# Performance work log

Hardware: AMD Instinct MI355X
Metric: run time of the kernel (lower is better)

## Reference

```python
import jax, jax.numpy as jnp
import numpy as np

N_GROUPS = 20   # hard-coded batch_size in NeRFGraph.forward
K = 3           # knn_graph k
IN_XYZ = 63
SKIP = 4
D = 8


def setup_inputs() -> dict:
    key = jax.random.key(0)
    B, W = 40960, 256
    G = B // N_GROUPS
    ks = jax.random.split(key, 22)

    def p(k, shape):
        fan_in = shape[-2] if len(shape) >= 2 else shape[-1]
        return jax.random.normal(k, shape, dtype=jnp.float32) / np.sqrt(fan_in)

    # batch assignment: exactly G nodes per group, randomly shuffled
    # (faithful to the np.zeros/fill/shuffle logic in the torch forward)
    batch_ids = jax.random.permutation(ks[1], jnp.repeat(jnp.arange(N_GROUPS, dtype=jnp.int32), G))

    return {
        "x": jax.random.normal(ks[0], (B, IN_XYZ + 27), dtype=jnp.float32),
        "batch_ids": batch_ids,
        "w0": p(ks[2], (IN_XYZ, W)), "b0": p(ks[3], (W,)),
        "w_mid": p(ks[4], (6, W, W)), "b_mid": p(ks[5], (6, W)),       # layers 1,2,3,5,6,7
        "w_skip": p(ks[6], (W + IN_XYZ, W)), "b_skip": p(ks[7], (W,)),  # layer 4 (skip)
        "w_final": p(ks[8], (W, W)), "b_final": p(ks[9], (W,)),
        "w_sigma": p(ks[10], (W, 1)), "b_sigma": p(ks[11], (1,)),
        "e1_w1": p(ks[12], (2 * (W + 27), W // 2)), "e1_b1": p(ks[13], (W // 2,)),
        "e1_w2": p(ks[14], (W // 2, W // 2)), "e1_b2": p(ks[15], (W // 2,)),
        "e2_w1": p(ks[16], (W, W // 2)), "e2_b1": p(ks[17], (W // 2,)),
        "e2_w2": p(ks[18], (W // 2, W // 2)), "e2_b2": p(ks[19], (W // 2,)),
        "w_rgb": p(ks[20], (W // 2, 3)), "b_rgb": p(ks[21], (3,)),
    }


def _knn(xyz, batch_ids):
    """k-NN within each of the N_GROUPS equal-size groups (loop=False).
    Returns (B, K) global neighbor indices for each node."""
    B = xyz.shape[0]
    G = B // N_GROUPS
    perm = jnp.argsort(batch_ids)                 # group nodes contiguously
    xg = xyz[perm].reshape(N_GROUPS, G, -1)
    sq = jnp.sum(xg * xg, axis=-1)                # (NG, G)
    d2 = sq[:, :, None] + sq[:, None, :] - 2.0 * jnp.einsum('gic,gjc->gij', xg, xg)
    d2 = jnp.where(jnp.eye(G, dtype=bool)[None], jnp.inf, d2)  # loop=False
    nbr_local = jax.lax.top_k(-d2, K)[1]          # (NG, G, K) local indices
    perm_g = perm.reshape(N_GROUPS, G)
    nbr_glob = jax.vmap(lambda p_, n_: p_[n_])(perm_g, nbr_local)  # (NG, G, K)
    inv = jnp.argsort(perm)
    return nbr_glob.reshape(B, K)[inv]


def _edge_conv(feat, nbr, w1, b1, w2, b2):
    # message: MLP(cat[x_i, x_j - x_i]); aggr='mean' over exactly K neighbors
    xi = feat[:, None, :]                         # (B, 1, C)
    xj = feat[nbr]                                # (B, K, C) gather
    tmp = jnp.concatenate([jnp.broadcast_to(xi, xj.shape), xj - xi], axis=-1)
    h = jax.nn.relu(tmp @ w1 + b1)
    h = jax.nn.relu(h @ w2 + b2)
    return h.mean(axis=1)                         # scatter-mean == mean over K


def reference(x, batch_ids, w0, b0, w_mid, b_mid, w_skip, b_skip, w_final, b_final,
              w_sigma, b_sigma, e1_w1, e1_b1, e1_w2, e1_b2, e2_w1, e2_b1, e2_w2, e2_b2,
              w_rgb, b_rgb):
    input_xyz, input_dir = x[:, :IN_XYZ], x[:, IN_XYZ:]
    nbr = _knn(input_xyz, batch_ids)
    h = jax.nn.relu(input_xyz @ w0 + b0)
    m = 0
    for i in range(1, D):
        if i == SKIP:
            h = jax.nn.relu(jnp.concatenate([input_xyz, h], axis=-1) @ w_skip + b_skip)
        else:
            h = jax.nn.relu(h @ w_mid[m] + b_mid[m])
            m += 1
    sigma = h @ w_sigma + b_sigma                  # (B, 1)
    feat = h @ w_final + b_final                   # xyz_encoding_final (no ReLU)
    d = _edge_conv(jnp.concatenate([feat, input_dir], axis=-1), nbr, e1_w1, e1_b1, e1_w2, e1_b2)
    d = _edge_conv(d, nbr, e2_w1, e2_b1, e2_w2, e2_b2)
    rgb = jax.nn.sigmoid(d @ w_rgb + b_rgb)        # (B, 3)
    return jnp.concatenate([rgb, sigma], axis=-1)  # (B, 4)
```

## Files before the change

kernel.cpp:

```cpp
#include <hip/hip_runtime.h>
#include <hip/hip_bf16.h>
#include <math.h>

#define B_TOTAL 40960
#define NGRP 20
#define GSZ 2048
#define CPART 4

typedef short short8 __attribute__((ext_vector_type(8)));
typedef short short4v __attribute__((ext_vector_type(4)));
typedef float f32x4 __attribute__((ext_vector_type(4)));
typedef float f32x16 __attribute__((ext_vector_type(16)));
typedef _Float16 half8 __attribute__((ext_vector_type(8)));
typedef _Float16 half4 __attribute__((ext_vector_type(4)));

__device__ __forceinline__ unsigned short bf16rne(float v)
{
    unsigned int u = __float_as_uint(v);
    unsigned int r = (u + 0x7FFFu + ((u >> 16) & 1u)) >> 16;
    return (unsigned short)r;
}

__device__ __forceinline__ float bf2f(unsigned short h)
{
    return __uint_as_float((unsigned int)h << 16);
}

__device__ __forceinline__ void splitf16(const float* v, half8& hi, half8& lo)
{
    #pragma unroll
    for (int j = 0; j < 8; j++) {
        _Float16 h = (_Float16)v[j];
        hi[j] = h;
        lo[j] = (_Float16)(v[j] - (float)h);
    }
}

__device__ __forceinline__ unsigned int fkey(float f)
{
    unsigned int u = __float_as_uint(f);
    unsigned int m = (unsigned int)((int)u >> 31) | 0x80000000u;
    return u ^ m;
}

__device__ __forceinline__ void ins3p(unsigned int k, unsigned int i,
    unsigned int& k0, unsigned int& i0, unsigned int& k1, unsigned int& i1,
    unsigned int& k2, unsigned int& i2)
{
    bool c0 = k < k0;
    unsigned int tk = c0 ? k0 : k, ti = c0 ? i0 : i;
    k0 = c0 ? k : k0;  i0 = c0 ? i : i0;
    bool c1 = tk < k1;
    unsigned int sk = c1 ? k1 : tk, si = c1 ? i1 : ti;
    k1 = c1 ? tk : k1; i1 = c1 ? ti : i1;
    bool c2 = sk < k2;
    k2 = c2 ? sk : k2; i2 = c2 ? si : i2;
}

__device__ __forceinline__ void mergerow(unsigned int& k0, unsigned int& i0,
    unsigned int& k1, unsigned int& i1, unsigned int& k2, unsigned int& i2)
{
    #pragma unroll
    for (int m = 1; m <= 8; m <<= 1) {
        unsigned int ok0 = (unsigned int)__shfl_xor((int)k0, m);
        unsigned int oi0 = (unsigned int)__shfl_xor((int)i0, m);
        unsigned int ok1 = (unsigned int)__shfl_xor((int)k1, m);
        unsigned int oi1 = (unsigned int)__shfl_xor((int)i1, m);
        unsigned int ok2 = (unsigned int)__shfl_xor((int)k2, m);
        unsigned int oi2 = (unsigned int)__shfl_xor((int)i2, m);
        ins3p(ok0, oi0, k0, i0, k1, i1, k2, i2);
        ins3p(ok1, oi1, k0, i0, k1, i1, k2, i2);
        ins3p(ok2, oi2, k0, i0, k1, i1, k2, i2);
    }
}

__global__ __launch_bounds__(1024) void k_scatter_det(const int* __restrict__ bid,
                                                      int* __restrict__ grp)
{
    __shared__ int cnts[640];
    __shared__ int offs[640];
    const int tid = threadIdx.x;
    const int w = tid >> 6, lane = tid & 63;
    const int g = blockIdx.x;
    for (int c = 0; c < 40; c++) {
        int i = c * 1024 + tid;
        unsigned long long m = __ballot(bid[i] == g);
        if (lane == 0) cnts[c * 16 + w] = __popcll(m);
    }
    __syncthreads();
    if (w == 0) {
        int base = lane * 10;
        int loc[10];
        int s = 0;
        #pragma unroll
        for (int u = 0; u < 10; u++) { loc[u] = s; s += cnts[base + u]; }
        int incl = s;
        #pragma unroll
        for (int d = 1; d < 64; d <<= 1) {
            int t = __shfl_up(incl, d);
            if (lane >= d) incl += t;
        }
        int excl = incl - s;
        #pragma unroll
        for (int u = 0; u < 10; u++) offs[base + u] = excl + loc[u];
    }
    __syncthreads();
    for (int c = 0; c < 40; c++) {
        int i = c * 1024 + tid;
        bool f = (bid[i] == g);
        unsigned long long m = __ballot(f);
        unsigned long long below = (lane == 0) ? 0ull : (m << (64 - lane)) >> (64 - lane);
        below = m & ((lane == 63) ? 0x7FFFFFFFFFFFFFFFull : ((1ull << lane) - 1ull));
        if (f) grp[g * GSZ + offs[c * 16 + w] + __popcll(below)] = i;
    }
}

__device__ __forceinline__ void do_wprep_trunk(int t, const float* __restrict__ w0,
    const float* __restrict__ wmid, const float* __restrict__ wskip,
    const float* __restrict__ wfin, _Float16* __restrict__ wfrag)
{
    const int CUMa[10] = {0,4,20,36,52,72,88,104,120,136};
    const int KCa[9]   = {4,16,16,16,20,16,16,16,16};
    int q = t >> 12;
    int L = 0;
    #pragma unroll
    for (int i = 0; i < 9; i++) if (q >= CUMa[i + 1]) L = i + 1;
    int cum = 0, kcn = 16;
    #pragma unroll
    for (int i = 0; i < 9; i++) if (L == i) { cum = CUMa[i]; kcn = KCa[i]; }
    int u = t - (cum << 12);
    int j = u & 7, lane = (u >> 3) & 63;
    int ckk = u >> 9;
    int kc = ckk % kcn, ct = ckk / kcn;
    int col = ct * 32 + (lane & 31);
    int k = kc * 16 + ((lane >> 5) << 3) + j;
    float w;
    if (L == 0)      w = (k < 63)  ? w0[k * 256 + col] : 0.f;
    else if (L == 4) w = (k < 256) ? wskip[(63 + k) * 256 + col]
                       : (k < 319) ? wskip[(k - 256) * 256 + col] : 0.f;
    else if (L == 8) w = wfin[k * 256 + col];
    else {
        int m = (L <= 3) ? (L - 1) : (L - 2);
        w = wmid[(size_t)m * 65536 + k * 256 + col];
    }
    wfrag[((size_t)cum << 12) + (size_t)ckk * 512 + lane * 8 + j] = (_Float16)w;
}

__device__ __forceinline__ void do_wprep_pq(int t, const float* __restrict__ src,
    int K, int KCN, _Float16* __restrict__ dst)
{
    int j = t & 7, lane = (t >> 3) & 63;
    int ckk = t >> 9;
    int kc = ckk % KCN, ct = ckk / KCN;
    int col = ct * 32 + (lane & 31);
    int k = kc * 16 + ((lane >> 5) << 3) + j;
    float w = 0.f;
    if (k < K) w = (col < 128) ? src[(size_t)k * 128 + col]
                               : src[(size_t)(K + k) * 128 + (col - 128)];
    dst[(size_t)ckk * 512 + lane * 8 + j] = (_Float16)w;
}

__device__ __forceinline__ void do_wprep_sq(int t, const float* __restrict__ src,
    _Float16* __restrict__ dst)
{
    int j = t & 7, lane = (t >> 3) & 63;
// ... 10 lines not shown
                       const float* __restrict__ e1w1, _Float16* __restrict__ wfpq1,
                       const float* __restrict__ e2w1, _Float16* __restrict__ wfpq2,
                       const float* __restrict__ e1w2, _Float16* __restrict__ wfe1,
                       const float* __restrict__ e2w2, _Float16* __restrict__ wfe2)
{
    const int b = blockIdx.x;
    const int tid = threadIdx.x;
    if (b < 2176) {
        do_wprep_trunk(b * 256 + tid, w0, wmid, wskip, wfin, wfrag);
    } else if (b < 2464) {
        do_wprep_pq((b - 2176) * 256 + tid, e1w1, 283, 18, wfpq1);
    } else if (b < 2592) {
        do_wprep_pq((b - 2464) * 256 + tid, e2w1, 128, 8, wfpq2);
    } else if (b < 2656) {
        do_wprep_sq((b - 2592) * 256 + tid, e1w2, wfe1);
    } else {
        do_wprep_sq((b - 2656) * 256 + tid, e2w2, wfe2);
    }
}

__global__ __launch_bounds__(256) void k_gather(const float* __restrict__ x,
    const int* __restrict__ grp, unsigned short* __restrict__ xbh,
    unsigned short* __restrict__ xbl, float* __restrict__ cn)
{
    __shared__ float tile[128][65];
    __shared__ int ids[128];
    const int tid = threadIdx.x;
    const int g = blockIdx.y;
    const int q0 = blockIdx.x * 128;
    if (tid < 128) ids[tid] = grp[g * GSZ + q0 + tid];
    __syncthreads();
    for (int s = tid; s < 128 * 64; s += 256) {
        int q = s >> 6, d = s & 63;
        tile[q][d] = (d < 63) ? x[(size_t)ids[q] * 90 + d] : 0.f;
    }
    __syncthreads();
    if (tid < 128) {
        float a = 0.f;
        #pragma unroll
        for (int d = 0; d < 63; d++) a = fmaf(tile[tid][d], tile[tid][d], a);
        cn[g * GSZ + q0 + tid] = a;
    }
    for (int s = tid; s < 128 * 32; s += 256) {
        int q = s >> 5, dp = (s & 31) << 1;
        float v0 = tile[q][dp], v1 = tile[q][dp + 1];
        unsigned short h0 = bf16rne(v0), h1 = bf16rne(v1);
        unsigned short l0 = bf16rne(v0 - bf2f(h0)), l1 = bf16rne(v1 - bf2f(h1));
        size_t pt = (size_t)g * GSZ + q0 + q;
        ((unsigned int*)xbh)[pt * 32 + (dp >> 1)] = (unsigned int)h0 | ((unsigned int)h1 << 16);
        ((unsigned int*)xbl)[pt * 32 + (dp >> 1)] = (unsigned int)l0 | ((unsigned int)l1 << 16);
    }
}

__global__ __launch_bounds__(256) void k_knn_mfma(const unsigned short* __restrict__ xbh,
    const unsigned short* __restrict__ xbl, const float* __restrict__ cn,
    unsigned long long* __restrict__ pkey)
{
    __shared__ char cbuf[2][16384];
    const int tid = threadIdx.x;
    const int lane = tid & 63;
    const int wave = tid >> 6;
    const int g = blockIdx.z;
    const int part = blockIdx.y;
    const int qt0 = blockIdx.x * 64 + wave * 16;
    const size_t gbase = (size_t)g * GSZ;
    const int lp = lane & 15;
    const int kgrp = lane >> 4;
    const int kg = kgrp << 3;

    const size_t qb = (gbase + qt0 + lp) * 64;
    short8 ah0 = *(const short8*)(xbh + qb + kg);
    short8 ah1 = *(const short8*)(xbh + qb + 32 + kg);
    short8 al0 = *(const short8*)(xbl + qb + kg);
    short8 al1 = *(const short8*)(xbl + qb + 32 + kg);

    const int qp0 = qt0 + (kgrp << 2);

    unsigned int K00 = ~0u, I00 = 0, K01 = ~0u, I01 = 0, K02 = ~0u, I02 = 0;
    unsigned int K10 = ~0u, I10 = 0, K11 = ~0u, I11 = 0, K12 = ~0u, I12 = 0;
    unsigned int K20 = ~0u, I20 = 0, K21 = ~0u, I21 = 0, K22 = ~0u, I22 = 0;
    unsigned int K30 = ~0u, I30 = 0, K31 = ~0u, I31 = 0, K32 = ~0u, I32 = 0;

    const int scand = tid & 63;
    const int cbeg = part * (GSZ / CPART);
    const int s0 = wave, s1 = 4 + wave, s2 = 8 + wave, s3 = 12 + wave;
    const unsigned short* pl0 = (s0 < 8) ? xbh : xbl;
    const unsigned short* pl1 = (s1 < 8) ? xbh : xbl;
    const unsigned short* pl2 = (s2 < 8) ? xbh : xbl;
    const unsigned short* pl3 = (s3 < 8) ? xbh : xbl;

    short8 st0, st1, st2, st3;
    {
        size_t cb = (gbase + cbeg + scand) * 64;
        st0 = *(const short8*)(pl0 + cb + (s0 & 7) * 8);
        st1 = *(const short8*)(pl1 + cb + (s1 & 7) * 8);
        st2 = *(const short8*)(pl2 + cb + (s2 & 7) * 8);
        st3 = *(const short8*)(pl3 + cb + (s3 & 7) * 8);
    }
    *(short8*)&cbuf[0][(s0 << 10) + (scand << 4)] = st0;
    *(short8*)&cbuf[0][(s1 << 10) + (scand << 4)] = st1;
    *(short8*)&cbuf[0][(s2 << 10) + (scand << 4)] = st2;
    *(short8*)&cbuf[0][(s3 << 10) + (scand << 4)] = st3;

    for (int ch = 0; ch < 8; ch++) {
        const int cur = ch & 1;
        __syncthreads();
        if (ch < 7) {
            size_t cb = (gbase + cbeg + (ch + 1) * 64 + scand) * 64;
            st0 = *(const short8*)(pl0 + cb + (s0 & 7) * 8);
            st1 = *(const short8*)(pl1 + cb + (s1 & 7) * 8);
            st2 = *(const short8*)(pl2 + cb + (s2 & 7) * 8);
            st3 = *(const short8*)(pl3 + cb + (s3 & 7) * 8);
        }
        const int cc0 = cbeg + ch * 64;
        #pragma unroll
        for (int ct = 0; ct < 4; ct++) {
            const int coff = ((ct * 16 + lp) << 4);
            short8 bh0 = *(const short8*)&cbuf[cur][((kgrp)      << 10) + coff];
            short8 bh1 = *(const short8*)&cbuf[cur][((4 + kgrp)  << 10) + coff];
            short8 bl0 = *(const short8*)&cbuf[cur][((8 + kgrp)  << 10) + coff];
            short8 bl1 = *(const short8*)&cbuf[cur][((12 + kgrp) << 10) + coff];
            f32x4 acc = {0.f, 0.f, 0.f, 0.f};
            acc = __builtin_amdgcn_mfma_f32_16x16x32_bf16(ah0, bh0, acc, 0, 0, 0);
            acc = __builtin_amdgcn_mfma_f32_16x16x32_bf16(ah1, bh1, acc, 0, 0, 0);
            acc = __builtin_amdgcn_mfma_f32_16x16x32_bf16(al0, bh0, acc, 0, 0, 0);
            acc = __builtin_amdgcn_mfma_f32_16x16x32_bf16(al1, bh1, acc, 0, 0, 0);
            acc = __builtin_amdgcn_mfma_f32_16x16x32_bf16(ah0, bl0, acc, 0, 0, 0);
            acc = __builtin_amdgcn_mfma_f32_16x16x32_bf16(ah1, bl1, acc, 0, 0, 0);
            const float cnv = cn[gbase + cc0 + ct * 16 + lp];
            const int cpos = cc0 + ct * 16 + lp;
            const unsigned int ci = (unsigned int)cpos;
            {
                unsigned int k = fkey(fmaf(-2.f, acc[0], cnv));
                k = (cpos == qp0 + 0) ? 0xFFFFFFFFu : k;
                ins3p(k, ci, K00, I00, K01, I01, K02, I02);
            }
            {
                unsigned int k = fkey(fmaf(-2.f, acc[1], cnv));
                k = (cpos == qp0 + 1) ? 0xFFFFFFFFu : k;
                ins3p(k, ci, K10, I10, K11, I11, K12, I12);
            }
            {
                unsigned int k = fkey(fmaf(-2.f, acc[2], cnv));
                k = (cpos == qp0 + 2) ? 0xFFFFFFFFu : k;
                ins3p(k, ci, K20, I20, K21, I21, K22, I22);
            }
            {
                unsigned int k = fkey(fmaf(-2.f, acc[3], cnv));
                k = (cpos == qp0 + 3) ? 0xFFFFFFFFu : k;
                ins3p(k, ci, K30, I30, K31, I31, K32, I32);
            }
        }
        if (ch < 7) {
            *(short8*)&cbuf[cur ^ 1][(s0 << 10) + (scand << 4)] = st0;
            *(short8*)&cbuf[cur ^ 1][(s1 << 10) + (scand << 4)] = st1;
            *(short8*)&cbuf[cur ^ 1][(s2 << 10) + (scand << 4)] = st2;
            *(short8*)&cbuf[cur ^ 1][(s3 << 10) + (scand << 4)] = st3;
        }
    }

    mergerow(K00, I00, K01, I01, K02, I02);
    mergerow(K10, I10, K11, I11, K12, I12);
    mergerow(K20, I20, K21, I21, K22, I22);
    mergerow(K30, I30, K31, I31, K32, I32);

    if (lp == 0) {
        size_t ob = (gbase + (size_t)qp0) * (CPART * 3) + part * 3;
        pkey[ob + 0]  = ((unsigned long long)K00 << 32) | I00;
        pkey[ob + 1]  = ((unsigned long long)K01 << 32) | I01;
        pkey[ob + 2]  = ((unsigned long long)K02 << 32) | I02;
        pkey[ob + 12] = ((unsigned long long)K10 << 32) | I10;
        pkey[ob + 13] = ((unsigned long long)K11 << 32) | I11;
        pkey[ob + 14] = ((unsigned long long)K12 << 32) | I12;
        pkey[ob + 24] = ((unsigned long long)K20 << 32) | I20;
        pkey[ob + 25] = ((unsigned long long)K21 << 32) | I21;
        pkey[ob + 26] = ((unsigned long long)K22 << 32) | I22;
        pkey[ob + 36] = ((unsigned long long)K30 << 32) | I30;
        pkey[ob + 37] = ((unsigned long long)K31 << 32) | I31;
        pkey[ob + 38] = ((unsigned long long)K32 << 32) | I32;
    }
}

__device__ __forceinline__ void ins3u(unsigned long long k,
    unsigned long long& k0, unsigned long long& k1, unsigned long long& k2)
{
    if (k < k0)      { k2 = k1; k1 = k0; k0 = k; }
    else if (k < k1) { k2 = k1; k1 = k; }
    else if (k < k2) { k2 = k; }
}

__global__ void k_knn_merge(const unsigned long long* __restrict__ pkey,
                            const int* __restrict__ grp, int* __restrict__ nbr)
{
    int t = blockIdx.x * 256 + threadIdx.x;
    if (t >= NGRP * GSZ) return;
    int g = t >> 11;
    unsigned long long k0 = ~0ull, k1 = ~0ull, k2 = ~0ull;
    const unsigned long long* pk = pkey + (size_t)t * (CPART * 3);
    #pragma unroll
    for (int r = 0; r < CPART * 3; r++) ins3u(pk[r], k0, k1, k2);
    int qi = grp[t];
    nbr[(size_t)qi * 3 + 0] = grp[(g << 11) + (int)(k0 & 0xFFFFFFFFull)];
    nbr[(size_t)qi * 3 + 1] = grp[(g << 11) + (int)(k1 & 0xFFFFFFFFull)];
    nbr[(size_t)qi * 3 + 2] = grp[(g << 11) + (int)(k2 & 0xFFFFFFFFull)];
}

template<int KCH, int KCX, int OUTMODE>
__device__ __forceinline__ void mlayer64(_Float16 (*Hh)[264], _Float16 (*Hl)[264],
    int rowbase, const float* __restrict__ x, const _Float16* __restrict__ wl,
    const float* __restrict__ bias, int lane, int wave)
{
    const int r31 = lane & 31, g = lane >> 5;
    constexpr int KC = KCH + KCX;
    const int ct = wave;
    f32x16 acc0, acc1;
    #pragma unroll
    for (int r = 0; r < 16; r++) { acc0[r] = 0.f; acc1[r] = 0.f; }
    const _Float16* wp = wl + (size_t)ct * KC * 512 + lane * 8;
    #pragma unroll
    for (int kc = 0; kc < KCH; kc++) {
        half8 ah0 = *(const half8*)&Hh[r31][kc * 16 + g * 8];
        half8 al0 = *(const half8*)&Hl[r31][kc * 16 + g * 8];
        half8 ah1 = *(const half8*)&Hh[32 + r31][kc * 16 + g * 8];
        half8 al1 = *(const half8*)&Hl[32 + r31][kc * 16 + g * 8];
        half8 b = *(const half8*)(wp + kc * 512);
        acc0 = __builtin_amdgcn_mfma_f32_32x32x16_f16(ah0, b, acc0, 0, 0, 0);
        acc1 = __builtin_amdgcn_mfma_f32_32x32x16_f16(ah1, b, acc1, 0, 0, 0);
        acc0 = __builtin_amdgcn_mfma_f32_32x32x16_f16(al0, b, acc0, 0, 0, 0);
        acc1 = __builtin_amdgcn_mfma_f32_32x32x16_f16(al1, b, acc1, 0, 0, 0);
    }
    #pragma unroll
    for (int t = 0; t < KCX; t++) {
        const int kc = KCH + t;
        float v0[8], v1[8];
        #pragma unroll
        for (int j = 0; j < 8; j++) {
            int kx = t * 16 + g * 8 + j;
            v0[j] = (kx < 63) ? x[(size_t)(rowbase + r31) * 90 + kx] : 0.f;
            v1[j] = (kx < 63) ? x[(size_t)(rowbase + 32 + r31) * 90 + kx] : 0.f;
        }
        half8 xh0, xl0, xh1, xl1;
        splitf16(v0, xh0, xl0);
        splitf16(v1, xh1, xl1);
        half8 b = *(const half8*)(wp + kc * 512);
        acc0 = __builtin_amdgcn_mfma_f32_32x32x16_f16(xh0, b, acc0, 0, 0, 0);
        acc1 = __builtin_amdgcn_mfma_f32_32x32x16_f16(xh1, b, acc1, 0, 0, 0);
        acc0 = __builtin_amdgcn_mfma_f32_32x32x16_f16(xl0, b, acc0, 0, 0, 0);
        acc1 = __builtin_amdgcn_mfma_f32_32x32x16_f16(xl1, b, acc1, 0, 0, 0);
    }
    const float bv = bias[ct * 32 + r31];
    __syncthreads();
    #pragma unroll
    for (int r = 0; r < 16; r++) {
        int row = (r & 3) + 8 * (r >> 2) + 4 * g;
        float v0 = acc0[r] + bv;
        float v1 = acc1[r] + bv;
        if (OUTMODE == 0) { v0 = fmaxf(v0, 0.f); v1 = fmaxf(v1, 0.f); }
        _Float16 h0 = (_Float16)v0, h1 = (_Float16)v1;
        Hh[row][ct * 32 + r31] = h0;
        Hl[row][ct * 32 + r31] = (_Float16)(v0 - (float)h0);
        Hh[32 + row][ct * 32 + r31] = h1;
        Hl[32 + row][ct * 32 + r31] = (_Float16)(v1 - (float)h1);
    }
    __syncthreads();
}

__global__ __launch_bounds__(512, 4) void k_trunk_mfma(const float* __restrict__ x,
    const _Float16* __restrict__ wfrag,
    const float* __restrict__ b0, const float* __restrict__ bmid,
    const float* __restrict__ bskip, const float* __restrict__ bfin,
    const float* __restrict__ wsig, const float* __restrict__ bsig,
    const _Float16* __restrict__ wfpq1, float* __restrict__ PQ,
    float* __restrict__ out)
{
    __shared__ _Float16 Hh[64][264];
    __shared__ _Float16 Hl[64][264];
    __shared__ _Float16 Dh[64][40];
    __shared__ _Float16 Dl[64][40];
    const int tid = threadIdx.x;
    const int lane = tid & 63;
    const int wave = tid >> 6;
    const int r31 = lane & 31, g = lane >> 5;
    const int rowbase = blockIdx.x * 64;
    for (int s = tid; s < 64 * 32; s += 512) {
        int r = s >> 5, d = s & 31;
        float v = (d < 27) ? x[(size_t)(rowbase + r) * 90 + 63 + d] : 0.f;
        _Float16 h = (_Float16)v;
        Dh[r][d] = h;
        Dl[r][d] = (_Float16)(v - (float)h);
    }
    const _Float16* W = wfrag;
    mlayer64<0, 4, 0>(Hh, Hl, rowbase, x, W + (size_t)0   * 4096, b0,          lane, wave);
    mlayer64<16,0, 0>(Hh, Hl, rowbase, x, W + (size_t)4   * 4096, bmid + 0,    lane, wave);
    mlayer64<16,0, 0>(Hh, Hl, rowbase, x, W + (size_t)20  * 4096, bmid + 256,  lane, wave);
    mlayer64<16,0, 0>(Hh, Hl, rowbase, x, W + (size_t)36  * 4096, bmid + 512,  lane, wave);
    mlayer64<16,4, 0>(Hh, Hl, rowbase, x, W + (size_t)52  * 4096, bskip,       lane, wave);
    mlayer64<16,0, 0>(Hh, Hl, rowbase, x, W + (size_t)72  * 4096, bmid + 768,  lane, wave);
    mlayer64<16,0, 0>(Hh, Hl, rowbase, x, W + (size_t)88  * 4096, bmid + 1024, lane, wave);
    mlayer64<16,0, 0>(Hh, Hl, rowbase, x, W + (size_t)104 * 4096, bmid + 1280, lane, wave);
    if (wave < 2) {
        const int row = wave * 32 + r31;
        float s = 0.f;
        #pragma unroll
        for (int kk = 0; kk < 32; kk++) {
            half4 hh = *(const half4*)&Hh[row][g * 128 + kk * 4];
            half4 hl = *(const half4*)&Hl[row][g * 128 + kk * 4];
            float4 wv = *(const float4*)&wsig[g * 128 + kk * 4];
            s = fmaf((float)hh[0] + (float)hl[0], wv.x, s);
            s = fmaf((float)hh[1] + (float)hl[1], wv.y, s);
            s = fmaf((float)hh[2] + (float)hl[2], wv.z, s);
            s = fmaf((float)hh[3] + (float)hl[3], wv.w, s);
        }
        s += __shfl_xor(s, 32);
        if (lane < 32) out[(size_t)(rowbase + row) * 4 + 3] = s + bsig[0];
    }
    mlayer64<16,0, 2>(Hh, Hl, rowbase, x, W + (size_t)120 * 4096, bfin, lane, wave);
    {
        const int ct = wave;
        f32x16 p0, p1;
        #pragma unroll
        for (int r = 0; r < 16; r++) { p0[r] = 0.f; p1[r] = 0.f; }
        const _Float16* wp = wfpq1 + (size_t)ct * 18 * 512 + lane * 8;
        #pragma unroll
        for (int kc = 0; kc < 16; kc++) {
            half8 ah0 = *(const half8*)&Hh[r31][kc * 16 + g * 8];
            half8 al0 = *(const half8*)&Hl[r31][kc * 16 + g * 8];
            half8 ah1 = *(const half8*)&Hh[32 + r31][kc * 16 + g * 8];
            half8 al1 = *(const half8*)&Hl[32 + r31][kc * 16 + g * 8];
            half8 b = *(const half8*)(wp + kc * 512);
            p0 = __builtin_amdgcn_mfma_f32_32x32x16_f16(ah0, b, p0, 0, 0, 0);
            p1 = __builtin_amdgcn_mfma_f32_32x32x16_f16(ah1, b, p1, 0, 0, 0);
            p0 = __builtin_amdgcn_mfma_f32_32x32x16_f16(al0, b, p0, 0, 0, 0);
            p1 = __builtin_amdgcn_mfma_f32_32x32x16_f16(al1, b, p1, 0, 0, 0);
        }
        #pragma unroll
        for (int kc = 16; kc < 18; kc++) {
            const int dc = (kc - 16) * 16 + g * 8;
            half8 ah0 = *(const half8*)&Dh[r31][dc];
            half8 al0 = *(const half8*)&Dl[r31][dc];
            half8 ah1 = *(const half8*)&Dh[32 + r31][dc];
            half8 al1 = *(const half8*)&Dl[32 + r31][dc];
            half8 b = *(const half8*)(wp + kc * 512);
            p0 = __builtin_amdgcn_mfma_f32_32x32x16_f16(ah0, b, p0, 0, 0, 0);
            p1 = __builtin_amdgcn_mfma_f32_32x32x16_f16(ah1, b, p1, 0, 0, 0);
            p0 = __builtin_amdgcn_mfma_f32_32x32x16_f16(al0, b, p0, 0, 0, 0);
            p1 = __builtin_amdgcn_mfma_f32_32x32x16_f16(al1, b, p1, 0, 0, 0);
        }
        #pragma unroll
        for (int r = 0; r < 16; r++) {
            int row = (r & 3) + 8 * (r >> 2) + 4 * g;
            PQ[(size_t)(rowbase + row) * 256 + ct * 32 + r31] = p0[r];
            PQ[(size_t)(rowbase + 32 + row) * 256 + ct * 32 + r31] = p1[r];
        }
    }
}

template<int RGB>
__global__ __launch_bounds__(256) void k_edge_mfma(const float* __restrict__ PQ,
    const float* __restrict__ b1, const _Float16* __restrict__ wf2,
    const float* __restrict__ b2, const int* __restrict__ nbr,
    const _Float16* __restrict__ wfpq2, float* __restrict__ pqout,
    const float* __restrict__ wrgb, const float* __restrict__ brgb,
    float* __restrict__ out)
{
    __shared__ _Float16 Hh[128][136];
    __shared__ _Float16 Hl[128][136];
    const int tid = threadIdx.x;
    const int lane = tid & 63, wave = tid >> 6;
    const int r31 = lane & 31, g = lane >> 5;
    const int n0 = blockIdx.x * 32;

    for (int s = tid; s < 128 * 32; s += 256) {
        int e = s >> 5, c4 = (s & 31) << 2;
        int n = e >> 2, jj = e & 3;
        half4 zh = {(_Float16)0.f, (_Float16)0.f, (_Float16)0.f, (_Float16)0.f};
        if (jj < 3) {
            int i = n0 + n;
            int j = nbr[(size_t)i * 3 + jj];
            float4 p  = *(const float4*)&PQ[(size_t)i * 256 + c4];
            float4 qi = *(const float4*)&PQ[(size_t)i * 256 + 128 + c4];
            float4 qj = *(const float4*)&PQ[(size_t)j * 256 + 128 + c4];
            float4 bv = *(const float4*)&b1[c4];
            float v[4];
            v[0] = fmaxf(p.x + bv.x + qj.x - qi.x, 0.f);
            v[1] = fmaxf(p.y + bv.y + qj.y - qi.y, 0.f);
            v[2] = fmaxf(p.z + bv.z + qj.z - qi.z, 0.f);
            v[3] = fmaxf(p.w + bv.w + qj.w - qi.w, 0.f);
            half4 hh, hl;
            #pragma unroll
            for (int u = 0; u < 4; u++) {
                _Float16 h = (_Float16)v[u];
                hh[u] = h;
                hl[u] = (_Float16)(v[u] - (float)h);
            }
            *(half4*)&Hh[e][c4] = hh;
            *(half4*)&Hl[e][c4] = hl;
        } else {
            *(half4*)&Hh[e][c4] = zh;
            *(half4*)&Hl[e][c4] = zh;
        }
    }
    __syncthreads();

    const int ct = wave;
    f32x16 a0, a1, a2, a3;
    #pragma unroll
    for (int r = 0; r < 16; r++) { a0[r] = 0.f; a1[r] = 0.f; a2[r] = 0.f; a3[r] = 0.f; }
// ... 87 lines not shown
    }
}

extern "C" void kernel_launch(void* const* d_in, const int* in_sizes, int n_in,
                              void* d_out, int out_size, void* d_ws, size_t ws_size,
                              hipStream_t stream)
{
    const float* x     = (const float*)d_in[0];
    const int*   bid   = (const int*)d_in[1];
    const float* w0    = (const float*)d_in[2];
    const float* b0    = (const float*)d_in[3];
    const float* wmid  = (const float*)d_in[4];
    const float* bmid  = (const float*)d_in[5];
    const float* wskip = (const float*)d_in[6];
    const float* bskip = (const float*)d_in[7];
    const float* wfin  = (const float*)d_in[8];
    const float* bfin  = (const float*)d_in[9];
    const float* wsig  = (const float*)d_in[10];
    const float* bsig  = (const float*)d_in[11];
    const float* e1w1  = (const float*)d_in[12];
    const float* e1b1  = (const float*)d_in[13];
    const float* e1w2  = (const float*)d_in[14];
    const float* e1b2  = (const float*)d_in[15];
    const float* e2w1  = (const float*)d_in[16];
    const float* e2b1  = (const float*)d_in[17];
    const float* e2w2  = (const float*)d_in[18];
    const float* e2b2  = (const float*)d_in[19];
    const float* wrgb  = (const float*)d_in[20];
    const float* brgb  = (const float*)d_in[21];
    float* out = (float*)d_out;

    char* ws = (char*)d_ws;
    int* grp = (int*)(ws + 256);
    int* nbr = (int*)(ws + 164096);
    _Float16* wfpq1 = (_Float16*)(ws + 655616);
    _Float16* wfpq2 = (_Float16*)(ws + 950528);
    _Float16* wfe1  = (_Float16*)(ws + 1081600);
    _Float16* wfe2  = (_Float16*)(ws + 1147136);
    float* bufA = (float*)(ws + (2 << 20));
    float* bufB = bufA + (size_t)B_TOTAL * 256;

    unsigned short* xbh = (unsigned short*)bufA;
    unsigned short* xbl = xbh + (size_t)B_TOTAL * 64;
    float* cn   = (float*)(xbl + (size_t)B_TOTAL * 64);
    unsigned long long* pkey = (unsigned long long*)(cn + B_TOTAL);
    _Float16* wfrag = (_Float16*)((char*)bufA + ((size_t)20 << 20));
    float* PQ  = bufB;
    float* PQ2 = bufA;

    k_prep<<<2720, 256, 0, stream>>>(w0, wmid, wskip, wfin, wfrag,
                                     e1w1, wfpq1, e2w1, wfpq2, e1w2, wfe1, e2w2, wfe2);
    k_scatter_det<<<NGRP, 1024, 0, stream>>>(bid, grp);
    k_gather<<<dim3(GSZ / 128, NGRP), 256, 0, stream>>>(x, grp, xbh, xbl, cn);
    k_knn_mfma<<<dim3(GSZ / 64, CPART, NGRP), 256, 0, stream>>>(xbh, xbl, cn, pkey);
    k_knn_merge<<<(NGRP * GSZ + 255) / 256, 256, 0, stream>>>(pkey, grp, nbr);
    k_trunk_mfma<<<B_TOTAL / 64, 512, 0, stream>>>(x, wfrag, b0, bmid, bskip, bfin,
                                                   wsig, bsig, wfpq1, PQ, out);
    k_edge_mfma<0><<<B_TOTAL / 32, 256, 0, stream>>>(PQ, e1b1, wfe1, e1b2, nbr,
                                                     wfpq2, PQ2, nullptr, nullptr, nullptr);
    k_edge_mfma<1><<<B_TOTAL / 32, 256, 0, stream>>>(PQ2, e2b1, wfe2, e2b2, nbr,
                                                     nullptr, nullptr, wrgb, brgb, out);
}
```

Baseline: 347.3 us.

## Merge kNN and trunk MLP into one heterogeneous launch to run concurrently

```diff
diff --git a/kernel.cpp b/kernel.cpp
--- a/kernel.cpp
+++ b/kernel.cpp
@@ -8,7 +8,6 @@
 #define CPART 4
 
 typedef short short8 __attribute__((ext_vector_type(8)));
-typedef short short4v __attribute__((ext_vector_type(4)));
 typedef float f32x4 __attribute__((ext_vector_type(4)));
 typedef float f32x16 __attribute__((ext_vector_type(16)));
 typedef _Float16 half8 __attribute__((ext_vector_type(8)));
@@ -109,8 +108,8 @@
         int i = c * 1024 + tid;
         bool f = (bid[i] == g);
         unsigned long long m = __ballot(f);
-        unsigned long long below = (lane == 0) ? 0ull : (m << (64 - lane)) >> (64 - lane);
-        below = m & ((lane == 63) ? 0x7FFFFFFFFFFFFFFFull : ((1ull << lane) - 1ull));
+        unsigned long long below = m & ((lane == 63) ? 0x7FFFFFFFFFFFFFFFull
+                                                     : ((1ull << lane) - 1ull));
         if (f) grp[g * GSZ + offs[c * 16 + w] + __popcll(below)] = i;
     }
 }
@@ -227,159 +226,6 @@
     }
 }
 
-__global__ __launch_bounds__(256) void k_knn_mfma(const unsigned short* __restrict__ xbh,
-    const unsigned short* __restrict__ xbl, const float* __restrict__ cn,
-    unsigned long long* __restrict__ pkey)
-{
-    __shared__ char cbuf[2][16384];
-    const int tid = threadIdx.x;
-    const int lane = tid & 63;
-    const int wave = tid >> 6;
-    const int g = blockIdx.z;
-    const int part = blockIdx.y;
-    const int qt0 = blockIdx.x * 64 + wave * 16;
-    const size_t gbase = (size_t)g * GSZ;
-    const int lp = lane & 15;
-    const int kgrp = lane >> 4;
-    const int kg = kgrp << 3;
-
-    const size_t qb = (gbase + qt0 + lp) * 64;
-    short8 ah0 = *(const short8*)(xbh + qb + kg);
-    short8 ah1 = *(const short8*)(xbh + qb + 32 + kg);
-    short8 al0 = *(const short8*)(xbl + qb + kg);
-    short8 al1 = *(const short8*)(xbl + qb + 32 + kg);
-
-    const int qp0 = qt0 + (kgrp << 2);
-
-    unsigned int K00 = ~0u, I00 = 0, K01 = ~0u, I01 = 0, K02 = ~0u, I02 = 0;
-    unsigned int K10 = ~0u, I10 = 0, K11 = ~0u, I11 = 0, K12 = ~0u, I12 = 0;
-    unsigned int K20 = ~0u, I20 = 0, K21 = ~0u, I21 = 0, K22 = ~0u, I22 = 0;
-    unsigned int K30 = ~0u, I30 = 0, K31 = ~0u, I31 = 0, K32 = ~0u, I32 = 0;
-
-    const int scand = tid & 63;
-    const int cbeg = part * (GSZ / CPART);
-    const int s0 = wave, s1 = 4 + wave, s2 = 8 + wave, s3 = 12 + wave;
-    const unsigned short* pl0 = (s0 < 8) ? xbh : xbl;
-    const unsigned short* pl1 = (s1 < 8) ? xbh : xbl;
-    const unsigned short* pl2 = (s2 < 8) ? xbh : xbl;
-    const unsigned short* pl3 = (s3 < 8) ? xbh : xbl;
-
-    short8 st0, st1, st2, st3;
-    {
-        size_t cb = (gbase + cbeg + scand) * 64;
-        st0 = *(const short8*)(pl0 + cb + (s0 & 7) * 8);
-        st1 = *(const short8*)(pl1 + cb + (s1 & 7) * 8);
-        st2 = *(const short8*)(pl2 + cb + (s2 & 7) * 8);
-        st3 = *(const short8*)(pl3 + cb + (s3 & 7) * 8);
-    }
-    *(short8*)&cbuf[0][(s0 << 10) + (scand << 4)] = st0;
-    *(short8*)&cbuf[0][(s1 << 10) + (scand << 4)] = st1;
-    *(short8*)&cbuf[0][(s2 << 10) + (scand << 4)] = st2;
-    *(short8*)&cbuf[0][(s3 << 10) + (scand << 4)] = st3;
-
-    for (int ch = 0; ch < 8; ch++) {
-        const int cur = ch & 1;
-        __syncthreads();
-        if (ch < 7) {
-            size_t cb = (gbase + cbeg + (ch + 1) * 64 + scand) * 64;
-            st0 = *(const short8*)(pl0 + cb + (s0 & 7) * 8);
-            st1 = *(const short8*)(pl1 + cb + (s1 & 7) * 8);
-            st2 = *(const short8*)(pl2 + cb + (s2 & 7) * 8);
-            st3 = *(const short8*)(pl3 + cb + (s3 & 7) * 8);
-        }
-        const int cc0 = cbeg + ch * 64;
-        #pragma unroll
-        for (int ct = 0; ct < 4; ct++) {
-            const int coff = ((ct * 16 + lp) << 4);
-            short8 bh0 = *(const short8*)&cbuf[cur][((kgrp)      << 10) + coff];
-            short8 bh1 = *(const short8*)&cbuf[cur][((4 + kgrp)  << 10) + coff];
-            short8 bl0 = *(const short8*)&cbuf[cur][((8 + kgrp)  << 10) + coff];
-            short8 bl1 = *(const short8*)&cbuf[cur][((12 + kgrp) << 10) + coff];
-            f32x4 acc = {0.f, 0.f, 0.f, 0.f};
-            acc = __builtin_amdgcn_mfma_f32_16x16x32_bf16(ah0, bh0, acc, 0, 0, 0);
-            acc = __builtin_amdgcn_mfma_f32_16x16x32_bf16(ah1, bh1, acc, 0, 0, 0);
-            acc = __builtin_amdgcn_mfma_f32_16x16x32_bf16(al0, bh0, acc, 0, 0, 0);
-            acc = __builtin_amdgcn_mfma_f32_16x16x32_bf16(al1, bh1, acc, 0, 0, 0);
-            acc = __builtin_amdgcn_mfma_f32_16x16x32_bf16(ah0, bl0, acc, 0, 0, 0);
-            acc = __builtin_amdgcn_mfma_f32_16x16x32_bf16(ah1, bl1, acc, 0, 0, 0);
-            const float cnv = cn[gbase + cc0 + ct * 16 + lp];
-            const int cpos = cc0 + ct * 16 + lp;
-            const unsigned int ci = (unsigned int)cpos;
-            {
-                unsigned int k = fkey(fmaf(-2.f, acc[0], cnv));
-                k = (cpos == qp0 + 0) ? 0xFFFFFFFFu : k;
-                ins3p(k, ci, K00, I00, K01, I01, K02, I02);
-            }
-            {
-                unsigned int k = fkey(fmaf(-2.f, acc[1], cnv));
-                k = (cpos == qp0 + 1) ? 0xFFFFFFFFu : k;
-                ins3p(k, ci, K10, I10, K11, I11, K12, I12);
-            }
-            {
-                unsigned int k = fkey(fmaf(-2.f, acc[2], cnv));
-                k = (cpos == qp0 + 2) ? 0xFFFFFFFFu : k;
-                ins3p(k, ci, K20, I20, K21, I21, K22, I22);
-            }
-            {
-                unsigned int k = fkey(fmaf(-2.f, acc[3], cnv));
-                k = (cpos == qp0 + 3) ? 0xFFFFFFFFu : k;
-                ins3p(k, ci, K30, I30, K31, I31, K32, I32);
-            }
-        }
-        if (ch < 7) {
-            *(short8*)&cbuf[cur ^ 1][(s0 << 10) + (scand << 4)] = st0;
-            *(short8*)&cbuf[cur ^ 1][(s1 << 10) + (scand << 4)] = st1;
-            *(short8*)&cbuf[cur ^ 1][(s2 << 10) + (scand << 4)] = st2;
-            *(short8*)&cbuf[cur ^ 1][(s3 << 10) + (scand << 4)] = st3;
-        }
-    }
-
-    mergerow(K00, I00, K01, I01, K02, I02);
-    mergerow(K10, I10, K11, I11, K12, I12);
-    mergerow(K20, I20, K21, I21, K22, I22);
-    mergerow(K30, I30, K31, I31, K32, I32);
-
-    if (lp == 0) {
-        size_t ob = (gbase + (size_t)qp0) * (CPART * 3) + part * 3;
-        pkey[ob + 0]  = ((unsigned long long)K00 << 32) | I00;
-        pkey[ob + 1]  = ((unsigned long long)K01 << 32) | I01;
-        pkey[ob + 2]  = ((unsigned long long)K02 << 32) | I02;
-        pkey[ob + 12] = ((unsigned long long)K10 << 32) | I10;
-        pkey[ob + 13] = ((unsigned long long)K11 << 32) | I11;
-        pkey[ob + 14] = ((unsigned long long)K12 << 32) | I12;
-        pkey[ob + 24] = ((unsigned long long)K20 << 32) | I20;
-        pkey[ob + 25] = ((unsigned long long)K21 << 32) | I21;
-        pkey[ob + 26] = ((unsigned long long)K22 << 32) | I22;
-        pkey[ob + 36] = ((unsigned long long)K30 << 32) | I30;
-        pkey[ob + 37] = ((unsigned long long)K31 << 32) | I31;
-        pkey[ob + 38] = ((unsigned long long)K32 << 32) | I32;
-    }
-}
-
-__device__ __forceinline__ void ins3u(unsigned long long k,
-    unsigned long long& k0, unsigned long long& k1, unsigned long long& k2)
-{
-    if (k < k0)      { k2 = k1; k1 = k0; k0 = k; }
-    else if (k < k1) { k2 = k1; k1 = k; }
-    else if (k < k2) { k2 = k; }
-}
-
-__global__ void k_knn_merge(const unsigned long long* __restrict__ pkey,
-                            const int* __restrict__ grp, int* __restrict__ nbr)
-{
-    int t = blockIdx.x * 256 + threadIdx.x;
-    if (t >= NGRP * GSZ) return;
-    int g = t >> 11;
-    unsigned long long k0 = ~0ull, k1 = ~0ull, k2 = ~0ull;
-    const unsigned long long* pk = pkey + (size_t)t * (CPART * 3);
-    #pragma unroll
-    for (int r = 0; r < CPART * 3; r++) ins3u(pk[r], k0, k1, k2);
-    int qi = grp[t];
-    nbr[(size_t)qi * 3 + 0] = grp[(g << 11) + (int)(k0 & 0xFFFFFFFFull)];
-    nbr[(size_t)qi * 3 + 1] = grp[(g << 11) + (int)(k1 & 0xFFFFFFFFull)];
-    nbr[(size_t)qi * 3 + 2] = grp[(g << 11) + (int)(k2 & 0xFFFFFFFFull)];
-}
-
 template<int KCH, int KCX, int OUTMODE>
 __device__ __forceinline__ void mlayer64(_Float16 (*Hh)[264], _Float16 (*Hl)[264],
     int rowbase, const float* __restrict__ x, const _Float16* __restrict__ wl,
@@ -440,94 +286,236 @@
     __syncthreads();
 }
 
-__global__ __launch_bounds__(512, 4) void k_trunk_mfma(const float* __restrict__ x,
+__global__ __launch_bounds__(512, 4) void k_main(const float* __restrict__ x,
     const _Float16* __restrict__ wfrag,
     const float* __restrict__ b0, const float* __restrict__ bmid,
     const float* __restrict__ bskip, const float* __restrict__ bfin,
     const float* __restrict__ wsig, const float* __restrict__ bsig,
     const _Float16* __restrict__ wfpq1, float* __restrict__ PQ,
-    float* __restrict__ out)
-{
-    __shared__ _Float16 Hh[64][264];
-    __shared__ _Float16 Hl[64][264];
-    __shared__ _Float16 Dh[64][40];
-    __shared__ _Float16 Dl[64][40];
+    float* __restrict__ out,
+    const unsigned short* __restrict__ xbh, const unsigned short* __restrict__ xbl,
+    const float* __restrict__ cn, unsigned long long* __restrict__ pkey)
+{
+    __shared__ union SM {
+        struct { _Float16 Hh[64][264]; _Float16 Hl[64][264];
+                 _Float16 Dh[64][40];  _Float16 Dl[64][40]; } t;
+        char knn[2][16384];
+    } sm;
     const int tid = threadIdx.x;
     const int lane = tid & 63;
     const int wave = tid >> 6;
     const int r31 = lane & 31, g = lane >> 5;
-    const int rowbase = blockIdx.x * 64;
-    for (int s = tid; s < 64 * 32; s += 512) {
-        int r = s >> 5, d = s & 31;
-        float v = (d < 27) ? x[(size_t)(rowbase + r) * 90 + 63 + d] : 0.f;
-        _Float16 h = (_Float16)v;
-        Dh[r][d] = h;
-        Dl[r][d] = (_Float16)(v - (float)h);
-    }
-    const _Float16* W = wfrag;
-    mlayer64<0, 4, 0>(Hh, Hl, rowbase, x, W + (size_t)0   * 4096, b0,          lane, wave);
-    mlayer64<16,0, 0>(Hh, Hl, rowbase, x, W + (size_t)4   * 4096, bmid + 0,    lane, wave);
-    mlayer64<16,0, 0>(Hh, Hl, rowbase, x, W + (size_t)20  * 4096, bmid + 256,  lane, wave);
-    mlayer64<16,0, 0>(Hh, Hl, rowbase, x, W + (size_t)36  * 4096, bmid + 512,  lane, wave);
-    mlayer64<16,4, 0>(Hh, Hl, rowbase, x, W + (size_t)52  * 4096, bskip,       lane, wave);
-    mlayer64<16,0, 0>(Hh, Hl, rowbase, x, W + (size_t)72  * 4096, bmid + 768,  lane, wave);
-    mlayer64<16,0, 0>(Hh, Hl, rowbase, x, W + (size_t)88  * 4096, bmid + 1024, lane, wave);
-    mlayer64<16,0, 0>(Hh, Hl, rowbase, x, W + (size_t)104 * 4096, bmid + 1280, lane, wave);
-    if (wave < 2) {
-        const int row = wave * 32 + r31;
-        float s = 0.f;
-        #pragma unroll
-        for (int kk = 0; kk < 32; kk++) {
-            half4 hh = *(const half4*)&Hh[row][g * 128 + kk * 4];
-            half4 hl = *(const half4*)&Hl[row][g * 128 + kk * 4];
-            float4 wv = *(const float4*)&wsig[g * 128 + kk * 4];
-            s = fmaf((float)hh[0] + (float)hl[0], wv.x, s);
-            s = fmaf((float)hh[1] + (float)hl[1], wv.y, s);
-            s = fmaf((float)hh[2] + (float)hl[2], wv.z, s);
-            s = fmaf((float)hh[3] + (float)hl[3], wv.w, s);
-        }
-        s += __shfl_xor(s, 32);
-        if (lane < 32) out[(size_t)(rowbase + row) * 4 + 3] = s + bsig[0];
-    }
-    mlayer64<16,0, 2>(Hh, Hl, rowbase, x, W + (size_t)120 * 4096, bfin, lane, wave);
-    {
-        const int ct = wave;
-        f32x16 p0, p1;
-        #pragma unroll
-        for (int r = 0; r < 16; r++) { p0[r] = 0.f; p1[r] = 0.f; }
-        const _Float16* wp = wfpq1 + (size_t)ct * 18 * 512 + lane * 8;
-        #pragma unroll
-        for (int kc = 0; kc < 16; kc++) {
-            half8 ah0 = *(const half8*)&Hh[r31][kc * 16 + g * 8];
-            half8 al0 = *(const half8*)&Hl[r31][kc * 16 + g * 8];
-            half8 ah1 = *(const half8*)&Hh[32 + r31][kc * 16 + g * 8];
-            half8 al1 = *(const half8*)&Hl[32 + r31][kc * 16 + g * 8];
-            half8 b = *(const half8*)(wp + kc * 512);
-            p0 = __builtin_amdgcn_mfma_f32_32x32x16_f16(ah0, b, p0, 0, 0, 0);
-            p1 = __builtin_amdgcn_mfma_f32_32x32x16_f16(ah1, b, p1, 0, 0, 0);
-            p0 = __builtin_amdgcn_mfma_f32_32x32x16_f16(al0, b, p0, 0, 0, 0);
-            p1 = __builtin_amdgcn_mfma_f32_32x32x16_f16(al1, b, p1, 0, 0, 0);
-        }
-        #pragma unroll
-        for (int kc = 16; kc < 18; kc++) {
-            const int dc = (kc - 16) * 16 + g * 8;
-            half8 ah0 = *(const half8*)&Dh[r31][dc];
-            half8 al0 = *(const half8*)&Dl[r31][dc];
-            half8 ah1 = *(const half8*)&Dh[32 + r31][dc];
-            half8 al1 = *(const half8*)&Dl[32 + r31][dc];
-            half8 b = *(const half8*)(wp + kc * 512);
-            p0 = __builtin_amdgcn_mfma_f32_32x32x16_f16(ah0, b, p0, 0, 0, 0);
-            p1 = __builtin_amdgcn_mfma_f32_32x32x16_f16(ah1, b, p1, 0, 0, 0);
-            p0 = __builtin_amdgcn_mfma_f32_32x32x16_f16(al0, b, p0, 0, 0, 0);
-            p1 = __builtin_amdgcn_mfma_f32_32x32x16_f16(al1, b, p1, 0, 0, 0);
-        }
-        #pragma unroll
-        for (int r = 0; r < 16; r++) {
-            int row = (r & 3) + 8 * (r >> 2) + 4 * g;
-            PQ[(size_t)(rowbase + row) * 256 + ct * 32 + r31] = p0[r];
-            PQ[(size_t)(rowbase + 32 + row) * 256 + ct * 32 + r31] = p1[r];
-        }
-    }
+
+    if (blockIdx.x < 640) {
+        const int rowbase = blockIdx.x * 64;
+        _Float16 (*Hh)[264] = sm.t.Hh;
+        _Float16 (*Hl)[264] = sm.t.Hl;
+        for (int s = tid; s < 64 * 32; s += 512) {
+            int r = s >> 5, d = s & 31;
+            float v = (d < 27) ? x[(size_t)(rowbase + r) * 90 + 63 + d] : 0.f;
+            _Float16 h = (_Float16)v;
+            sm.t.Dh[r][d] = h;
+            sm.t.Dl[r][d] = (_Float16)(v - (float)h);
+        }
+        const _Float16* W = wfrag;
+        mlayer64<0, 4, 0>(Hh, Hl, rowbase, x, W + (size_t)0   * 4096, b0,          lane, wave);
+        mlayer64<16,0, 0>(Hh, Hl, rowbase, x, W + (size_t)4   * 4096, bmid + 0,    lane, wave);
+        mlayer64<16,0, 0>(Hh, Hl, rowbase, x, W + (size_t)20  * 4096, bmid + 256,  lane, wave);
+        mlayer64<16,0, 0>(Hh, Hl, rowbase, x, W + (size_t)36  * 4096, bmid + 512,  lane, wave);
+        mlayer64<16,4, 0>(Hh, Hl, rowbase, x, W + (size_t)52  * 4096, bskip,       lane, wave);
+        mlayer64<16,0, 0>(Hh, Hl, rowbase, x, W + (size_t)72  * 4096, bmid + 768,  lane, wave);
+        mlayer64<16,0, 0>(Hh, Hl, rowbase, x, W + (size_t)88  * 4096, bmid + 1024, lane, wave);
+        mlayer64<16,0, 0>(Hh, Hl, rowbase, x, W + (size_t)104 * 4096, bmid + 1280, lane, wave);
+        if (wave < 2) {
+            const int row = wave * 32 + r31;
+            float s = 0.f;
+            #pragma unroll
+            for (int kk = 0; kk < 32; kk++) {
+                half4 hh = *(const half4*)&Hh[row][g * 128 + kk * 4];
+                half4 hl = *(const half4*)&Hl[row][g * 128 + kk * 4];
+                float4 wv = *(const float4*)&wsig[g * 128 + kk * 4];
+                s = fmaf((float)hh[0] + (float)hl[0], wv.x, s);
+                s = fmaf((float)hh[1] + (float)hl[1], wv.y, s);
+                s = fmaf((float)hh[2] + (float)hl[2], wv.z, s);
+                s = fmaf((float)hh[3] + (float)hl[3], wv.w, s);
+            }
+            s += __shfl_xor(s, 32);
+            if (lane < 32) out[(size_t)(rowbase + row) * 4 + 3] = s + bsig[0];
+        }
+        mlayer64<16,0, 2>(Hh, Hl, rowbase, x, W + (size_t)120 * 4096, bfin, lane, wave);
+        {
+            const int ct = wave;
+            f32x16 p0, p1;
+            #pragma unroll
+            for (int r = 0; r < 16; r++) { p0[r] = 0.f; p1[r] = 0.f; }
+            const _Float16* wp = wfpq1 + (size_t)ct * 18 * 512 + lane * 8;
+            #pragma unroll
+            for (int kc = 0; kc < 16; kc++) {
+                half8 ah0 = *(const half8*)&Hh[r31][kc * 16 + g * 8];
+                half8 al0 = *(const half8*)&Hl[r31][kc * 16 + g * 8];
+                half8 ah1 = *(const half8*)&Hh[32 + r31][kc * 16 + g * 8];
+                half8 al1 = *(const half8*)&Hl[32 + r31][kc * 16 + g * 8];
+                half8 b = *(const half8*)(wp + kc * 512);
+                p0 = __builtin_amdgcn_mfma_f32_32x32x16_f16(ah0, b, p0, 0, 0, 0);
+                p1 = __builtin_amdgcn_mfma_f32_32x32x16_f16(ah1, b, p1, 0, 0, 0);
+                p0 = __builtin_amdgcn_mfma_f32_32x32x16_f16(al0, b, p0, 0, 0, 0);
+                p1 = __builtin_amdgcn_mfma_f32_32x32x16_f16(al1, b, p1, 0, 0, 0);
+            }
+            #pragma unroll
+            for (int kc = 16; kc < 18; kc++) {
+                const int dc = (kc - 16) * 16 + g * 8;
+                half8 ah0 = *(const half8*)&sm.t.Dh[r31][dc];
+                half8 al0 = *(const half8*)&sm.t.Dl[r31][dc];
+                half8 ah1 = *(const half8*)&sm.t.Dh[32 + r31][dc];
+                half8 al1 = *(const half8*)&sm.t.Dl[32 + r31][dc];
+                half8 b = *(const half8*)(wp + kc * 512);
+                p0 = __builtin_amdgcn_mfma_f32_32x32x16_f16(ah0, b, p0, 0, 0, 0);
+                p1 = __builtin_amdgcn_mfma_f32_32x32x16_f16(ah1, b, p1, 0, 0, 0);
+                p0 = __builtin_amdgcn_mfma_f32_32x32x16_f16(al0, b, p0, 0, 0, 0);
+                p1 = __builtin_amdgcn_mfma_f32_32x32x16_f16(al1, b, p1, 0, 0, 0);
+            }
+            #pragma unroll
+            for (int r = 0; r < 16; r++) {
+                int row = (r & 3) + 8 * (r >> 2) + 4 * g;
+                PQ[(size_t)(rowbase + row) * 256 + ct * 32 + r31] = p0[r];
+                PQ[(size_t)(rowbase + 32 + row) * 256 + ct * 32 + r31] = p1[r];
+            }
+        }
+    } else {
+        const int bb = blockIdx.x - 640;
+        const int gg = bb >> 6;
+        const int rem = bb & 63;
+        const int part = rem >> 4;
+        const int qx = rem & 15;
+        const int qt0 = qx * 128 + wave * 16;
+        const size_t gbase = (size_t)gg * GSZ;
+        const int lp = lane & 15;
+        const int kgrp = lane >> 4;
+        const int kg = kgrp << 3;
+        char (*cbuf)[16384] = sm.knn;
+
+        const size_t qb = (gbase + qt0 + lp) * 64;
+        short8 ah0 = *(const short8*)(xbh + qb + kg);
+        short8 ah1 = *(const short8*)(xbh + qb + 32 + kg);
+        short8 al0 = *(const short8*)(xbl + qb + kg);
+        short8 al1 = *(const short8*)(xbl + qb + 32 + kg);
+
+        const int qp0 = qt0 + (kgrp << 2);
+
+        unsigned int K00 = ~0u, I00 = 0, K01 = ~0u, I01 = 0, K02 = ~0u, I02 = 0;
+        unsigned int K10 = ~0u, I10 = 0, K11 = ~0u, I11 = 0, K12 = ~0u, I12 = 0;
+        unsigned int K20 = ~0u, I20 = 0, K21 = ~0u, I21 = 0, K22 = ~0u, I22 = 0;
+        unsigned int K30 = ~0u, I30 = 0, K31 = ~0u, I31 = 0, K32 = ~0u, I32 = 0;
+
+        const int cbeg = part * (GSZ / CPART);
+
+        short8 st0, st1;
+        {
+            size_t cb = (gbase + cbeg + lane) * 64;
+            st0 = *(const short8*)(xbh + cb + wave * 8);
+            st1 = *(const short8*)(xbl + cb + wave * 8);
+        }
+        *(short8*)&cbuf[0][(wave << 10) + (lane << 4)] = st0;
+        *(short8*)&cbuf[0][((8 + wave) << 10) + (lane << 4)] = st1;
+
+        for (int ch = 0; ch < 8; ch++) {
+            const int cur = ch & 1;
+            __syncthreads();
+            if (ch < 7) {
+                size_t cb = (gbase + cbeg + (ch + 1) * 64 + lane) * 64;
+                st0 = *(const short8*)(xbh + cb + wave * 8);
+                st1 = *(const short8*)(xbl + cb + wave * 8);
+            }
+            const int cc0 = cbeg + ch * 64;
+            #pragma unroll
+            for (int ct = 0; ct < 4; ct++) {
+                const int coff = ((ct * 16 + lp) << 4);
+                short8 bh0 = *(const short8*)&cbuf[cur][((kgrp)      << 10) + coff];
+                short8 bh1 = *(const short8*)&cbuf[cur][((4 + kgrp)  << 10) + coff];
+                short8 bl0 = *(const short8*)&cbuf[cur][((8 + kgrp)  << 10) + coff];
+                short8 bl1 = *(const short8*)&cbuf[cur][((12 + kgrp) << 10) + coff];
+                f32x4 acc = {0.f, 0.f, 0.f, 0.f};
+                acc = __builtin_amdgcn_mfma_f32_16x16x32_bf16(ah0, bh0, acc, 0, 0, 0);
+                acc = __builtin_amdgcn_mfma_f32_16x16x32_bf16(ah1, bh1, acc, 0, 0, 0);
+                acc = __builtin_amdgcn_mfma_f32_16x16x32_bf16(al0, bh0, acc, 0, 0, 0);
+                acc = __builtin_amdgcn_mfma_f32_16x16x32_bf16(al1, bh1, acc, 0, 0, 0);
+                acc = __builtin_amdgcn_mfma_f32_16x16x32_bf16(ah0, bl0, acc, 0, 0, 0);
+                acc = __builtin_amdgcn_mfma_f32_16x16x32_bf16(ah1, bl1, acc, 0, 0, 0);
+                const float cnv = cn[gbase + cc0 + ct * 16 + lp];
+                const int cpos = cc0 + ct * 16 + lp;
+                const unsigned int ci = (unsigned int)cpos;
+                {
+                    unsigned int k = fkey(fmaf(-2.f, acc[0], cnv));
+                    k = (cpos == qp0 + 0) ? 0xFFFFFFFFu : k;
+                    ins3p(k, ci, K00, I00, K01, I01, K02, I02);
+                }
+                {
+                    unsigned int k = fkey(fmaf(-2.f, acc[1], cnv));
+                    k = (cpos == qp0 + 1) ? 0xFFFFFFFFu : k;
+                    ins3p(k, ci, K10, I10, K11, I11, K12, I12);
+                }
+                {
+                    unsigned int k = fkey(fmaf(-2.f, acc[2], cnv));
+                    k = (cpos == qp0 + 2) ? 0xFFFFFFFFu : k;
+                    ins3p(k, ci, K20, I20, K21, I21, K22, I22);
+                }
+                {
+                    unsigned int k = fkey(fmaf(-2.f, acc[3], cnv));
+                    k = (cpos == qp0 + 3) ? 0xFFFFFFFFu : k;
+                    ins3p(k, ci, K30, I30, K31, I31, K32, I32);
+                }
+            }
+            if (ch < 7) {
+                *(short8*)&cbuf[cur ^ 1][(wave << 10) + (lane << 4)] = st0;
+                *(short8*)&cbuf[cur ^ 1][((8 + wave) << 10) + (lane << 4)] = st1;
+            }
+        }
+
+        mergerow(K00, I00, K01, I01, K02, I02);
+        mergerow(K10, I10, K11, I11, K12, I12);
+        mergerow(K20, I20, K21, I21, K22, I22);
+        mergerow(K30, I30, K31, I31, K32, I32);
+
+        if (lp == 0) {
+            size_t ob = (gbase + (size_t)qp0) * (CPART * 3) + part * 3;
+            pkey[ob + 0]  = ((unsigned long long)K00 << 32) | I00;
+            pkey[ob + 1]  = ((unsigned long long)K01 << 32) | I01;
+            pkey[ob + 2]  = ((unsigned long long)K02 << 32) | I02;
+            pkey[ob + 12] = ((unsigned long long)K10 << 32) | I10;
+            pkey[ob + 13] = ((unsigned long long)K11 << 32) | I11;
+            pkey[ob + 14] = ((unsigned long long)K12 << 32) | I12;
+            pkey[ob + 24] = ((unsigned long long)K20 << 32) | I20;
+            pkey[ob + 25] = ((unsigned long long)K21 << 32) | I21;
+            pkey[ob + 26] = ((unsigned long long)K22 << 32) | I22;
+            pkey[ob + 36] = ((unsigned long long)K30 << 32) | I30;
+            pkey[ob + 37] = ((unsigned long long)K31 << 32) | I31;
+            pkey[ob + 38] = ((unsigned long long)K32 << 32) | I32;
+        }
+    }
+}
+
+__device__ __forceinline__ void ins3u(unsigned long long k,
+    unsigned long long& k0, unsigned long long& k1, unsigned long long& k2)
+{
+    if (k < k0)      { k2 = k1; k1 = k0; k0 = k; }
+    else if (k < k1) { k2 = k1; k1 = k; }
+    else if (k < k2) { k2 = k; }
+}
+
+__global__ void k_knn_merge(const unsigned long long* __restrict__ pkey,
+                            const int* __restrict__ grp, int* __restrict__ nbr)
+{
+    int t = blockIdx.x * 256 + threadIdx.x;
+    if (t >= NGRP * GSZ) return;
+    int g = t >> 11;
+    unsigned long long k0 = ~0ull, k1 = ~0ull, k2 = ~0ull;
+    const unsigned long long* pk = pkey + (size_t)t * (CPART * 3);
+    #pragma unroll
+    for (int r = 0; r < CPART * 3; r++) ins3u(pk[r], k0, k1, k2);
+    int qi = grp[t];
+    nbr[(size_t)qi * 3 + 0] = grp[(g << 11) + (int)(k0 & 0xFFFFFFFFull)];
+    nbr[(size_t)qi * 3 + 1] = grp[(g << 11) + (int)(k1 & 0xFFFFFFFFull)];
+    nbr[(size_t)qi * 3 + 2] = grp[(g << 11) + (int)(k2 & 0xFFFFFFFFull)];
 }
 
 template<int RGB>
@@ -721,10 +709,10 @@
                                      e1w1, wfpq1, e2w1, wfpq2, e1w2, wfe1, e2w2, wfe2);
     k_scatter_det<<<NGRP, 1024, 0, stream>>>(bid, grp);
     k_gather<<<dim3(GSZ / 128, NGRP), 256, 0, stream>>>(x, grp, xbh, xbl, cn);
-    k_knn_mfma<<<dim3(GSZ / 64, CPART, NGRP), 256, 0, stream>>>(xbh, xbl, cn, pkey);
+    k_main<<<640 + 1280, 512, 0, stream>>>(x, wfrag, b0, bmid, bskip, bfin,
+                                           wsig, bsig, wfpq1, PQ, out,
+                                           xbh, xbl, cn, pkey);
     k_knn_merge<<<(NGRP * GSZ + 255) / 256, 256, 0, stream>>>(pkey, grp, nbr);
-    k_trunk_mfma<<<B_TOTAL / 64, 512, 0, stream>>>(x, wfrag, b0, bmid, bskip, bfin,
-                                                   wsig, bsig, wfpq1, PQ, out);
     k_edge_mfma<0><<<B_TOTAL / 32, 256, 0, stream>>>(PQ, e1b1, wfe1, e1b2, nbr,
                                                      wfpq2, PQ2, nullptr, nullptr, nullptr);
     k_edge_mfma<1><<<B_TOTAL / 32, 256, 0, stream>>>(PQ2, e2b1, wfe2, e2b2, nbr,
```

Result: faster. 321.1 us (median of 2 runs) (-7.5%).
